# Kernel optimization log

Hardware: AMD Instinct MI355X
Metric: run time of the kernel (lower is better)

The kernel has to match this reference:

```python
import jax, jax.numpy as jnp
import numpy as np

N0, N1, N2 = 100000, 25000, 6250
E0, E1, E2 = 600000, 150000, 37500
K = 6


def cheb_conv(x, edge_index, W, b):
    """torch_geometric ChebConv with sym normalization, lambda_max=2:
    L_hat = -D^{-1/2} A D^{-1/2}; T0=x, T1=L_hat x, Tk=2 L_hat T_{k-1} - T_{k-2}."""
    n = x.shape[0]
    src, dst = edge_index[0], edge_index[1]
    deg = jax.ops.segment_sum(jnp.ones(src.shape[0], x.dtype), src, num_segments=n)
    dinv = jnp.where(deg > 0, jax.lax.rsqrt(jnp.maximum(deg, 1.0)), 0.0)
    w = -(dinv[src] * dinv[dst])  # [E]

    def prop(h):  # (L_hat h)_i = sum_{j->i} w_ij h_j
        return jax.ops.segment_sum(w[:, None] * h[src], dst, num_segments=n)

    Tx0 = x
    out = Tx0 @ W[0]
    Tx1 = prop(x)
    out = out + Tx1 @ W[1]
    for k in range(2, W.shape[0]):
        Tx2 = 2.0 * prop(Tx1) - Tx0
        out = out + Tx2 @ W[k]
        Tx0, Tx1 = Tx1, Tx2
    return out + b


def pool(x, rows, cols, vals, n_out):
    # sparse.mm(D, x): y[r] += v * x[c]
    return jax.ops.segment_sum(vals[:, None] * x[cols], rows, num_segments=n_out)


def setup_inputs() -> dict:
    key = jax.random.key(0)
    ks = jax.random.split(key, 16)
    inp = {}
    inp["x"] = jax.random.normal(ks[0], (N0, 3), jnp.float32)
    inp["edge_index0"] = jax.random.randint(ks[1], (2, E0), 0, N0, jnp.int32)
    inp["edge_index1"] = jax.random.randint(ks[2], (2, E1), 0, N1, jnp.int32)
    inp["edge_index2"] = jax.random.randint(ks[3], (2, E2), 0, N2, jnp.int32)
    s = 0.05
    inp["W0"] = jax.random.normal(ks[4], (K, 3, 128), jnp.float32) * s
    inp["b0"] = jax.random.normal(ks[5], (128,), jnp.float32) * s
    inp["W1"] = jax.random.normal(ks[6], (K, 128, 128), jnp.float32) * s
    inp["b1"] = jax.random.normal(ks[7], (128,), jnp.float32) * s
    inp["W2"] = jax.random.normal(ks[8], (K, 128, 256), jnp.float32) * s
    inp["b2"] = jax.random.normal(ks[9], (256,), jnp.float32) * s
    inp["D0_rows"] = jax.random.randint(ks[10], (100000,), 0, N1, jnp.int32)
    inp["D0_cols"] = jax.random.randint(ks[11], (100000,), 0, N0, jnp.int32)
    inp["D0_vals"] = jax.random.uniform(ks[12], (100000,), jnp.float32)
    inp["D1_rows"] = jax.random.randint(ks[13], (25000,), 0, N2, jnp.int32)
    inp["D1_cols"] = jax.random.randint(ks[14], (25000,), 0, N1, jnp.int32)
    inp["D1_vals"] = jax.random.uniform(ks[15], (25000,), jnp.float32)
    k2 = jax.random.split(jax.random.fold_in(key, 1), 2)
    inp["linW"] = jax.random.normal(k2[0], (10, N2 * 256), jnp.float32) * 0.001
    inp["linb"] = jax.random.normal(k2[1], (10,), jnp.float32) * s
    return inp


def reference(x, edge_index0, edge_index1, edge_index2, W0, b0, W1, b1, W2, b2,
              D0_rows, D0_cols, D0_vals, D1_rows, D1_cols, D1_vals, linW, linb):
    h = jax.nn.relu(cheb_conv(x, edge_index0, W0, b0))      # [N0,128]
    h = pool(h, D0_rows, D0_cols, D0_vals, N1)               # [N1,128]
    h = jax.nn.relu(cheb_conv(h, edge_index1, W1, b1))      # [N1,128]
    h = pool(h, D1_rows, D1_cols, D1_vals, N2)               # [N2,128]
    h = cheb_conv(h, edge_index2, W2, b2)                    # [N2,256]
    Z = linW @ h.reshape(-1) + linb                           # [10]
    return Z
```

## Files before the change

kernel.cpp:

```cpp
#include <hip/hip_runtime.h>


namespace {
constexpr int cN0 = 100000, cN1 = 25000, cN2 = 6250;
constexpr int cE0 = 600000, cE1 = 150000, cE2 = 37500;
constexpr int cD  = cN2 * 256;

constexpr int JN[8]  = {cN0, cN1, cN2, cN1, cN2, cN0, cN1, cN2};
constexpr int JE[8]  = {cE0, cE1, cE2, 100000, 25000, cE0, cE1, cE2};
constexpr int JB[8]  = {391, 98, 25, 98, 25, 391, 98, 25};
constexpr int JBBASE[9] = {0, 391, 489, 514, 612, 637, 1028, 1126, 1151};
constexpr int TB = 1151;
constexpr int JCB[8] = {293, 74, 19, 49, 13, 293, 74, 19};
constexpr int JCBASE[9] = {0, 293, 367, 386, 435, 448, 741, 815, 834};
constexpr int TCB = 834;
constexpr int CHUNK = 2048;
constexpr int BSTRIDE = 400;

constexpr int EBASE[5]   = {0, 600000, 750000, 787500, 887500};
constexpr int E_TOTAL    = 912500;
constexpr int SBASE[3]   = {0, 600000, 750000};
constexpr int S_TOTAL    = 787500;
constexpr int NBASE[5]   = {0, 100096, 125184, 131584, 156672};
constexpr int NPAD_TOTAL = 163072;
constexpr int DEGBASE[3] = {0, 100000, 125000};
constexpr int DEG_TOTAL  = 131250;
}

typedef __attribute__((ext_vector_type(8))) short short8;
typedef __attribute__((ext_vector_type(4))) float floatx4;

__device__ inline ushort f2bf(float f) {
  union { float f; unsigned u; } v; v.f = f;
  unsigned u = v.u;
  return (ushort)((u + 0x7FFFu + ((u >> 16) & 1u)) >> 16);
}

__device__ inline int job_of_cb(int cb) {
  int j = 0;
  while (cb >= JCBASE[j + 1]) ++j;
  return j;
}
__device__ inline int job_of_bucket(int g) {
  int j = 0;
  while (g >= JBBASE[j + 1]) ++j;
  return j;
}

__global__ __launch_bounds__(256) void c1_count_kernel(
    const int* __restrict__ k0, const int* __restrict__ k1, const int* __restrict__ k2,
    const int* __restrict__ k3, const int* __restrict__ k4, const int* __restrict__ k5,
    const int* __restrict__ k6, const int* __restrict__ k7,
    int* __restrict__ cntCB) {
  __shared__ int cnt[BSTRIDE];
  int cb = blockIdx.x;
  int j = job_of_cb(cb);
  int lb = cb - JCBASE[j];
  const int* keys;
  switch (j) {
    case 0: keys = k0; break; case 1: keys = k1; break; case 2: keys = k2; break;
    case 3: keys = k3; break; case 4: keys = k4; break; case 5: keys = k5; break;
    case 6: keys = k6; break; default: keys = k7; break;
  }
  int nB = JB[j];
  for (int b = threadIdx.x; b < nB; b += 256) cnt[b] = 0;
  __syncthreads();
  int e0 = lb * CHUNK;
  int e1 = min(e0 + CHUNK, JE[j]);
  for (int e = e0 + threadIdx.x; e < e1; e += 256)
    atomicAdd(&cnt[keys[e] >> 8], 1);
  __syncthreads();
  for (int b = threadIdx.x; b < nB; b += 256)
    cntCB[cb * BSTRIDE + b] = cnt[b];
}

__global__ __launch_bounds__(256) void c2a_scan_kernel(int* __restrict__ cntCB,
                                                       int* __restrict__ bucketTot) {
  __shared__ int s[256];
  int g = blockIdx.x;
  int j = job_of_bucket(g);
  int b = g - JBBASE[j];
  int cb0 = JCBASE[j], nCB = JCB[j];
  int carry = 0;
  for (int c0 = 0; c0 < nCB; c0 += 256) {
    int i = c0 + threadIdx.x;
    int v = (i < nCB) ? cntCB[(cb0 + i) * BSTRIDE + b] : 0;
    s[threadIdx.x] = v;
    __syncthreads();
    for (int d = 1; d < 256; d <<= 1) {
      int t = (threadIdx.x >= d) ? s[threadIdx.x - d] : 0;
      __syncthreads();
      s[threadIdx.x] += t;
      __syncthreads();
    }
    if (i < nCB) cntCB[(cb0 + i) * BSTRIDE + b] = carry + s[threadIdx.x] - v;
    carry += s[255];
    __syncthreads();
  }
  if (threadIdx.x == 0) bucketTot[g] = carry;
}

__global__ __launch_bounds__(256) void c2b_scan_kernel(const int* __restrict__ bucketTot,
                                                       int* __restrict__ bucketBase) {
  __shared__ int s[256];
  int j = blockIdx.x;
  int g0 = JBBASE[j], nB = JB[j];
  int carry = 0;
  for (int c0 = 0; c0 < nB; c0 += 256) {
    int i = c0 + threadIdx.x;
    int v = (i < nB) ? bucketTot[g0 + i] : 0;
    s[threadIdx.x] = v;
    __syncthreads();
    for (int d = 1; d < 256; d <<= 1) {
      int t = (threadIdx.x >= d) ? s[threadIdx.x - d] : 0;
      __syncthreads();
      s[threadIdx.x] += t;
      __syncthreads();
    }
    if (i < nB) bucketBase[g0 + i] = carry + s[threadIdx.x] - v;
    carry += s[255];
    __syncthreads();
  }
}

__global__ __launch_bounds__(256) void c3_src_kernel(
    const int* __restrict__ s0, const int* __restrict__ s1, const int* __restrict__ s2,
    const int* __restrict__ cntCB, const int* __restrict__ bucketBase,
    int* __restrict__ scatSrc) {
  __shared__ int base[BSTRIDE];
  int cb = blockIdx.x + JCBASE[5];
  int j = job_of_cb(cb);
  int lb = cb - JCBASE[j];
  const int* keys = (j == 5) ? s0 : (j == 6) ? s1 : s2;
  int nB = JB[j];
  for (int b = threadIdx.x; b < nB; b += 256)
    base[b] = SBASE[j - 5] + bucketBase[JBBASE[j] + b] + cntCB[cb * BSTRIDE + b];
  __syncthreads();
  int e0 = lb * CHUNK;
  int e1 = min(e0 + CHUNK, JE[j]);
  for (int e = e0 + threadIdx.x; e < e1; e += 256) {
    int s = keys[e];
    int pos = atomicAdd(&base[s >> 8], 1);
    scatSrc[pos] = s & 255;
  }
}

__global__ __launch_bounds__(256) void ddeg_kernel(const int* __restrict__ scatSrc,
                                                   const int* __restrict__ bucketTot,
                                                   const int* __restrict__ bucketBase,
                                                   float* __restrict__ dinv) {
  __shared__ int cnt[256];
  int g = blockIdx.x + JBBASE[5];
  int j = job_of_bucket(g);
  int b = g - JBBASE[j];
  int st = SBASE[j - 5] + bucketBase[g];
  int en = st + bucketTot[g];
  cnt[threadIdx.x] = 0;
  __syncthreads();
  for (int idx = st + threadIdx.x; idx < en; idx += 256)
    atomicAdd(&cnt[scatSrc[idx]], 1);
  __syncthreads();
  int node = b * 256 + threadIdx.x;
  if (node < JN[j]) {
    int c = cnt[threadIdx.x];
    dinv[DEGBASE[j - 5] + node] = (c > 0) ? rsqrtf((float)c) : 0.f;
  }
}

__global__ __launch_bounds__(256) void c3_dst_kernel(
    const int* __restrict__ d0, const int* __restrict__ s0,
    const int* __restrict__ d1, const int* __restrict__ s1,
    const int* __restrict__ d2, const int* __restrict__ s2,
    const int* __restrict__ p0r, const int* __restrict__ p0c, const float* __restrict__ p0v,
    const int* __restrict__ p1r, const int* __restrict__ p1c, const float* __restrict__ p1v,
    const float* __restrict__ dinv,
    const int* __restrict__ cntCB, const int* __restrict__ bucketBase,
    int2* __restrict__ scatPairs) {
  __shared__ int base[BSTRIDE];
  int cb = blockIdx.x;
  int j = job_of_cb(cb);
  int lb = cb - JCBASE[j];
  const int* dk; const int* sk; const float* vv = nullptr;
  switch (j) {
    case 0: dk = d0; sk = s0; break;
    case 1: dk = d1; sk = s1; break;
    case 2: dk = d2; sk = s2; break;
    case 3: dk = p0r; sk = p0c; vv = p0v; break;
    default: dk = p1r; sk = p1c; vv = p1v; break;
  }
  int nB = JB[j];
  for (int b = threadIdx.x; b < nB; b += 256)
    base[b] = EBASE[j] + bucketBase[JBBASE[j] + b] + cntCB[cb * BSTRIDE + b];
  __syncthreads();
  int e0 = lb * CHUNK;
  int e1 = min(e0 + CHUNK, JE[j]);
  for (int e = e0 + threadIdx.x; e < e1; e += 256) {
    int d = dk[e];
    int s = sk[e];
    float w;
    if (j < 3) w = -(dinv[DEGBASE[j] + s] * dinv[DEGBASE[j] + d]);
    else w = vv[e];
    int pos = atomicAdd(&base[d >> 8], 1);
    scatPairs[pos] = make_int2(((d & 255) << 17) | s, __float_as_int(w));
  }
}

__global__ __launch_bounds__(256) void dcsr_kernel(const int2* __restrict__ scatPairs,
                                                   const int* __restrict__ bucketTot,
                                                   const int* __restrict__ bucketBase,
                                                   int* __restrict__ off,
                                                   int2* __restrict__ csrPairs) {
  __shared__ int cnt[256];
  __shared__ int sArr[256];
  __shared__ int cur[256];
  int g = blockIdx.x;
  int j = job_of_bucket(g);
  int b = g - JBBASE[j];
  int relBase = bucketBase[g];
  int st = EBASE[j] + relBase;
  int en = st + bucketTot[g];
  cnt[threadIdx.x] = 0;
  __syncthreads();
  for (int idx = st + threadIdx.x; idx < en; idx += 256)
    atomicAdd(&cnt[scatPairs[idx].x >> 17], 1);
  __syncthreads();
  int v = cnt[threadIdx.x];
  sArr[threadIdx.x] = v;
  __syncthreads();
  for (int d = 1; d < 256; d <<= 1) {
    int t = (threadIdx.x >= d) ? sArr[threadIdx.x - d] : 0;
    __syncthreads();
    sArr[threadIdx.x] += t;
    __syncthreads();
  }
  int excl = sArr[threadIdx.x] - v;
  int node = b * 256 + threadIdx.x;
  if (node < JN[j]) off[NBASE[j] + node] = relBase + excl;
  if (threadIdx.x == 0 && b == JB[j] - 1) off[NBASE[j] + JN[j]] = JE[j];
  cur[threadIdx.x] = st + excl;
  __syncthreads();
  for (int idx = st + threadIdx.x; idx < en; idx += 256) {
    int2 p = scatPairs[idx];
    int dl = p.x >> 17;
    int s = p.x & 0x1FFFF;
    int pos = atomicAdd(&cur[dl], 1);
    csrPairs[pos] = make_int2(s, p.y);
  }
}

__global__ __launch_bounds__(256) void csr_prop128_kernel(
    const int* __restrict__ off, const int2* __restrict__ pairs,
    const float* __restrict__ h, float* __restrict__ y, ushort* __restrict__ ybf,
    const float* __restrict__ prev, float scale, int N) {
  int r = blockIdx.x * 8 + (threadIdx.x >> 5);
  int l = threadIdx.x & 31;
  if (r >= N) return;
  int s = off[r], e = off[r + 1];
  const float4* h4 = (const float4*)h;
  float ax = 0.f, ay = 0.f, az = 0.f, aw = 0.f;
  int j = s;
  for (; j + 4 <= e; j += 4) {
    int2 p0 = pairs[j], p1 = pairs[j + 1], p2 = pairs[j + 2], p3 = pairs[j + 3];
    float4 v0 = h4[(size_t)p0.x * 32 + l];
    float4 v1 = h4[(size_t)p1.x * 32 + l];
    float4 v2 = h4[(size_t)p2.x * 32 + l];
    float4 v3 = h4[(size_t)p3.x * 32 + l];
    float w0 = __int_as_float(p0.y), w1 = __int_as_float(p1.y);
    float w2 = __int_as_float(p2.y), w3 = __int_as_float(p3.y);
    ax += w0 * v0.x + w1 * v1.x + w2 * v2.x + w3 * v3.x;
    ay += w0 * v0.y + w1 * v1.y + w2 * v2.y + w3 * v3.y;
    az += w0 * v0.z + w1 * v1.z + w2 * v2.z + w3 * v3.z;
    aw += w0 * v0.w + w1 * v1.w + w2 * v2.w + w3 * v3.w;
  }
  for (; j < e; ++j) {
    int2 p = pairs[j];
    float4 v0 = h4[(size_t)p.x * 32 + l];
    float w = __int_as_float(p.y);
    ax += w * v0.x; ay += w * v0.y; az += w * v0.z; aw += w * v0.w;
  }
  float4 v = make_float4(scale * ax, scale * ay, scale * az, scale * aw);
  if (prev) {
    float4 pv = ((const float4*)prev)[(size_t)r * 32 + l];
    v.x -= pv.x; v.y -= pv.y; v.z -= pv.z; v.w -= pv.w;
  }
  if (y) ((float4*)y)[(size_t)r * 32 + l] = v;
  uint2 sp = make_uint2(f2bf(v.x) | ((unsigned)f2bf(v.y) << 16),
                        f2bf(v.z) | ((unsigned)f2bf(v.w) << 16));
  ((uint2*)ybf)[(size_t)r * 32 + l] = sp;
}

__global__ void csr_prop3_kernel(const int* __restrict__ off, const int2* __restrict__ pairs,
                                 const float4* __restrict__ T, float4* __restrict__ Tout,
                                 int kin, int kout, int kprev, float scale, int N) {
  int r = blockIdx.x * blockDim.x + threadIdx.x;
  if (r >= N) return;
  int s = off[r], e = off[r + 1];
  float ax = 0.f, ay = 0.f, az = 0.f;
  int j = s;
  for (; j + 4 <= e; j += 4) {
    int2 p0 = pairs[j], p1 = pairs[j + 1], p2 = pairs[j + 2], p3 = pairs[j + 3];
    float4 h0 = T[(size_t)p0.x * 6 + kin];
    float4 h1 = T[(size_t)p1.x * 6 + kin];
    float4 h2 = T[(size_t)p2.x * 6 + kin];
    float4 h3 = T[(size_t)p3.x * 6 + kin];
    float w0 = __int_as_float(p0.y), w1 = __int_as_float(p1.y);
    float w2 = __int_as_float(p2.y), w3 = __int_as_float(p3.y);
    ax += w0 * h0.x + w1 * h1.x + w2 * h2.x + w3 * h3.x;
    ay += w0 * h0.y + w1 * h1.y + w2 * h2.y + w3 * h3.y;
    az += w0 * h0.z + w1 * h1.z + w2 * h2.z + w3 * h3.z;
  }
  for (; j < e; ++j) {
    int2 p = pairs[j];
    float4 hv = T[(size_t)p.x * 6 + kin];
    float w = __int_as_float(p.y);
    ax += w * hv.x; ay += w * hv.y; az += w * hv.z;
  }
  float4 v = make_float4(scale * ax, scale * ay, scale * az, 0.f);
  if (kprev >= 0) {
    float4 pv = T[(size_t)r * 6 + kprev];
    v.x -= pv.x; v.y -= pv.y; v.z -= pv.z;
  }
  Tout[(size_t)r * 6 + kout] = v;
}

__global__ void copyx_kernel(const float* __restrict__ x, float4* __restrict__ Tb, int N) {
  int r = blockIdx.x * 256 + threadIdx.x;
  if (r < N) Tb[(size_t)r * 6] = make_float4(x[3 * r], x[3 * r + 1], x[3 * r + 2], 0.f);
}

__global__ __launch_bounds__(256) void g18pool_kernel(
    const int* __restrict__ off, const int2* __restrict__ pairs,
    const float4* __restrict__ Tb0, const float* __restrict__ W0,
    const float* __restrict__ b0, float* __restrict__ T0out,
    ushort* __restrict__ T0bf, int N) {
  int r = blockIdx.x * 2 + (threadIdx.x >> 7);
  int f = threadIdx.x & 127;
  float wcol[18];
#pragma unroll
  for (int t = 0; t < 18; ++t) wcol[t] = W0[t * 128 + f];
  float bv = b0[f];
  if (r >= N) return;
  int s = off[r], e = off[r + 1];
  float acc = 0.f;
  int j = s;
  for (; j + 2 <= e; j += 2) {
    int2 p0 = pairs[j], p1 = pairs[j + 1];
    const float4* t0 = Tb0 + (size_t)p0.x * 6;
    const float4* t1 = Tb0 + (size_t)p1.x * 6;
    float d0 = bv, d1 = bv;
#pragma unroll
    for (int k = 0; k < 6; ++k) {
      float4 a = t0[k];
      float4 b = t1[k];
      d0 += a.x * wcol[k * 3] + a.y * wcol[k * 3 + 1] + a.z * wcol[k * 3 + 2];
      d1 += b.x * wcol[k * 3] + b.y * wcol[k * 3 + 1] + b.z * wcol[k * 3 + 2];
    }
    acc += __int_as_float(p0.y) * fmaxf(d0, 0.f) + __int_as_float(p1.y) * fmaxf(d1, 0.f);
  }
  if (j < e) {
    int2 p = pairs[j];
    const float4* t0 = Tb0 + (size_t)p.x * 6;
    float d = bv;
#pragma unroll
    for (int k = 0; k < 6; ++k) {
      float4 a = t0[k];
      d += a.x * wcol[k * 3] + a.y * wcol[k * 3 + 1] + a.z * wcol[k * 3 + 2];
    }
    acc += __int_as_float(p.y) * fmaxf(d, 0.f);
  }
  T0out[(size_t)r * 128 + f] = acc;
  T0bf[(size_t)r * 128 + f] = f2bf(acc);
}

__global__ void prep_w_kernel(const float* __restrict__ W1, const float* __restrict__ W2,
                              ushort* __restrict__ Wt1, ushort* __restrict__ Wt2) {
  int i = blockIdx.x * 256 + threadIdx.x;
  if (i < 768 * 128) {
    int k = i / 128, n = i - k * 128;
    Wt1[(size_t)n * 768 + k] = f2bf(W1[i]);
  } else {
    int i2 = i - 768 * 128;
    if (i2 < 768 * 256) {
      int k = i2 / 256, n = i2 - k * 256;
      Wt2[(size_t)n * 768 + k] = f2bf(W2[i2]);
    }
  }
}

template <int RELU>
__global__ __launch_bounds__(256, 2) void gemm_mfma_kernel(
    const ushort* __restrict__ Tbf, const ushort* __restrict__ Wt,
    const float* __restrict__ bias, float* __restrict__ C, int M, int N) {
  __shared__ ushort Al[64][40];
  __shared__ ushort Bl[128][40];
  const int tid = threadIdx.x;
  const int rowBase = blockIdx.x * 64;
  const int colBase = blockIdx.y * 128;
  const int wave = tid >> 6;
  const int lane = tid & 63;
  const int m16 = lane & 15;
  const int quad = lane >> 4;
  const size_t Mstride = (size_t)M * 128;

  floatx4 acc[8];
#pragma unroll
  for (int c = 0; c < 8; ++c)
#pragma unroll
    for (int r = 0; r < 4; ++r) acc[c][r] = 0.f;

  const int sRow = tid >> 2;
  const int sK8 = (tid & 3) * 8;
  const int growA = rowBase + sRow;
  const bool aValid = growA < M;

  for (int kc = 0; kc < 24; ++kc) {
    uint4 av = make_uint4(0, 0, 0, 0);
    if (aValid)
      av = *(const uint4*)(Tbf + (size_t)(kc >> 2) * Mstride + (size_t)growA * 128
                           + ((kc & 3) << 5) + sK8);
    *(uint4*)&Al[sRow][sK8] = av;
#pragma unroll
    for (int l = 0; l < 2; ++l) {
      int lin = tid + l * 256;
      int bRow = lin >> 2;
      int bK8 = (lin & 3) * 8;
      *(uint4*)&Bl[bRow][bK8] =
          *(const uint4*)(Wt + (size_t)(colBase + bRow) * 768 + kc * 32 + bK8);
    }
    __syncthreads();

    short8 a = *(const short8*)&Al[wave * 16 + m16][quad * 8];
#pragma unroll
    for (int c = 0; c < 8; ++c) {
      short8 b = *(const short8*)&Bl[c * 16 + m16][quad * 8];
      acc[c] = __builtin_amdgcn_mfma_f32_16x16x32_bf16(a, b, acc[c], 0, 0, 0);
    }
    __syncthreads();
  }

#pragma unroll
  for (int c = 0; c < 8; ++c) {
    int col = colBase + c * 16 + m16;
    float bv = bias[col];
#pragma unroll
    for (int r = 0; r < 4; ++r) {
      int row = rowBase + wave * 16 + quad * 4 + r;
      if (row < M) {
        float v = acc[c][r] + bv;
        if (RELU) v = fmaxf(v, 0.f);
        C[(size_t)row * N + col] = v;
      }
    }
  }
}

__global__ void initout_kernel(float* __restrict__ out, const float* __restrict__ linb) {
  int i = threadIdx.x;
  if (i < 10) out[i] = linb[i];
}

__global__ __launch_bounds__(256) void linear_kernel(const float* __restrict__ Wl,
                                                     const float* __restrict__ h,
                                                     float* __restrict__ out, int D) {
  float p[10];
#pragma unroll
  for (int j = 0; j < 10; ++j) p[j] = 0.f;
  int stride = gridDim.x * blockDim.x;
  for (int i = blockIdx.x * blockDim.x + threadIdx.x; i < D; i += stride) {
    float hv = h[i];
#pragma unroll
    for (int j = 0; j < 10; ++j) p[j] += Wl[(size_t)j * D + i] * hv;
  }
#pragma unroll
  for (int j = 0; j < 10; ++j) {
#pragma unroll
    for (int off = 32; off > 0; off >>= 1) p[j] += __shfl_down(p[j], off, 64);
  }
  __shared__ float s[4][10];
  int wave = threadIdx.x >> 6, lane = threadIdx.x & 63;
  if (lane == 0) {
#pragma unroll
    for (int j = 0; j < 10; ++j) s[wave][j] = p[j];
  }
  __syncthreads();
  if (threadIdx.x < 10) {
    float t = s[0][threadIdx.x] + s[1][threadIdx.x] + s[2][threadIdx.x] + s[3][threadIdx.x];
    atomicAdd(&out[threadIdx.x], t);
  }
}

extern "C" void kernel_launch(void* const* d_in, const int* in_sizes, int n_in,
                              void* d_out, int out_size, void* d_ws, size_t ws_size,
                              hipStream_t stream) {
  const float* x    = (const float*)d_in[0];
  const int*   ei0  = (const int*)d_in[1];
  const int*   ei1  = (const int*)d_in[2];
  const int*   ei2  = (const int*)d_in[3];
  const float* W0   = (const float*)d_in[4];
  const float* b0   = (const float*)d_in[5];
  const float* W1   = (const float*)d_in[6];
  const float* b1   = (const float*)d_in[7];
  const float* W2   = (const float*)d_in[8];
  const float* b2   = (const float*)d_in[9];
  const int*   D0r  = (const int*)d_in[10];
  const int*   D0c  = (const int*)d_in[11];
  const float* D0v  = (const float*)d_in[12];
  const int*   D1r  = (const int*)d_in[13];
  const int*   D1c  = (const int*)d_in[14];
  const float* D1v  = (const float*)d_in[15];
  const float* linW = (const float*)d_in[16];
  const float* linb = (const float*)d_in[17];
  float* out = (float*)d_out;
  (void)in_sizes; (void)n_in; (void)out_size; (void)ws_size;

  const int* src0 = ei0;            const int* dst0 = ei0 + cE0;
  const int* src1 = ei1;            const int* dst1 = ei1 + cE1;
  const int* src2 = ei2;            const int* dst2 = ei2 + cE2;

  float* ws = (float*)d_ws;
  size_t off = 0;
  auto alloc = [&](size_t n) {
    float* p = ws + off;
    off += (n + 63) & ~size_t(63);
    return p;
  };
  float* dinv       = alloc(DEG_TOTAL);
  int*   cntCB      = (int*)alloc((size_t)TCB * BSTRIDE);
  int*   bucketTot  = (int*)alloc(TB);
  int*   bucketBase = (int*)alloc(TB);
  int*   scatSrc    = (int*)alloc(S_TOTAL);
  int2*  scatPairs  = (int2*)alloc((size_t)2 * E_TOTAL);
  int2*  csrPairs   = (int2*)alloc((size_t)2 * E_TOTAL);
  int*   offArr     = (int*)alloc(NPAD_TOTAL);
  ushort* Wt1       = (ushort*)alloc(768 * 128 / 2);
  ushort* Wt2       = (ushort*)alloc(768 * 256 / 2);
  float4* Tb0       = (float4*)alloc((size_t)cN0 * 24);
  float* Tlvl1      = alloc((size_t)6 * cN1 * 128);
  ushort* Tbf1      = (ushort*)alloc((size_t)6 * cN1 * 64);
  float* out1       = alloc((size_t)cN1 * 128);
  float* Tlvl2      = alloc((size_t)6 * cN2 * 128);
  ushort* Tbf2      = (ushort*)alloc((size_t)6 * cN2 * 64);
  float* out2       = alloc((size_t)cN2 * 256);

  auto nb = [](long long n) { return (unsigned)((n + 255) / 256); };

  c1_count_kernel<<<TCB, 256, 0, stream>>>(dst0, dst1, dst2, D0r, D1r,
                                           src0, src1, src2, cntCB);
  c2a_scan_kernel<<<TB, 256, 0, stream>>>(cntCB, bucketTot);
  c2b_scan_kernel<<<8, 256, 0, stream>>>(bucketTot, bucketBase);
  c3_src_kernel<<<TCB - JCBASE[5], 256, 0, stream>>>(src0, src1, src2,
                                                     cntCB, bucketBase, scatSrc);
  ddeg_kernel<<<TB - JBBASE[5], 256, 0, stream>>>(scatSrc, bucketTot, bucketBase, dinv);
  c3_dst_kernel<<<JCBASE[5], 256, 0, stream>>>(dst0, src0, dst1, src1, dst2, src2,
                                               D0r, D0c, D0v, D1r, D1c, D1v,
                                               dinv, cntCB, bucketBase, scatPairs);
  dcsr_kernel<<<JBBASE[5], 256, 0, stream>>>(scatPairs, bucketTot, bucketBase,
                                             offArr, csrPairs);
  prep_w_kernel<<<nb(768 * 384), 256, 0, stream>>>(W1, W2, Wt1, Wt2);

  auto seg_off   = [&](int s) { return offArr + NBASE[s]; };
  auto seg_pairs = [&](int s) { return csrPairs + EBASE[s]; };

  copyx_kernel<<<nb(cN0), 256, 0, stream>>>(x, Tb0, cN0);
  csr_prop3_kernel<<<nb(cN0), 256, 0, stream>>>(seg_off(0), seg_pairs(0),
      Tb0, Tb0, 0, 1, -1, 1.f, cN0);
  csr_prop3_kernel<<<nb(cN0), 256, 0, stream>>>(seg_off(0), seg_pairs(0),
      Tb0, Tb0, 1, 2, 0, 2.f, cN0);
  csr_prop3_kernel<<<nb(cN0), 256, 0, stream>>>(seg_off(0), seg_pairs(0),
      Tb0, Tb0, 2, 3, 1, 2.f, cN0);
  csr_prop3_kernel<<<nb(cN0), 256, 0, stream>>>(seg_off(0), seg_pairs(0),
      Tb0, Tb0, 3, 4, 2, 2.f, cN0);
  csr_prop3_kernel<<<nb(cN0), 256, 0, stream>>>(seg_off(0), seg_pairs(0),
      Tb0, Tb0, 4, 5, 3, 2.f, cN0);
  g18pool_kernel<<<(cN1 + 1) / 2, 256, 0, stream>>>(
      seg_off(3), seg_pairs(3), Tb0, W0, b0, Tlvl1, Tbf1, cN1);

  {
    auto Tk  = [&](int k) { return Tlvl1 + (size_t)k * cN1 * 128; };
    auto Tbk = [&](int k) { return Tbf1 + (size_t)k * cN1 * 128; };
    auto prop = [&](int kin, int kout, int kprev, float scale, bool needF32) {
      csr_prop128_kernel<<<(cN1 + 7) / 8, 256, 0, stream>>>(
          seg_off(1), seg_pairs(1), Tk(kin), needF32 ? Tk(kout) : nullptr, Tbk(kout),
          (kprev >= 0) ? Tk(kprev) : nullptr, scale, cN1);
    };
    prop(0, 1, -1, 1.f, true);
    prop(1, 2, 0, 2.f, true);
    prop(2, 3, 1, 2.f, true);
    prop(3, 4, 2, 2.f, true);
    prop(4, 5, 3, 2.f, false);
    dim3 g((cN1 + 63) / 64, 1);
    gemm_mfma_kernel<1><<<g, 256, 0, stream>>>(Tbf1, Wt1, b1, out1, cN1, 128);
  }

  csr_prop128_kernel<<<(cN2 + 7) / 8, 256, 0, stream>>>(
      seg_off(4), seg_pairs(4), out1, Tlvl2, Tbf2, nullptr, 1.f, cN2);

  {
    auto Tk  = [&](int k) { return Tlvl2 + (size_t)k * cN2 * 128; };
    auto Tbk = [&](int k) { return Tbf2 + (size_t)k * cN2 * 128; };
    auto prop = [&](int kin, int kout, int kprev, float scale, bool needF32) {
      csr_prop128_kernel<<<(cN2 + 7) / 8, 256, 0, stream>>>(
          seg_off(2), seg_pairs(2), Tk(kin), needF32 ? Tk(kout) : nullptr, Tbk(kout),
          (kprev >= 0) ? Tk(kprev) : nullptr, scale, cN2);
    };
    prop(0, 1, -1, 1.f, true);
    prop(1, 2, 0, 2.f, true);
    prop(2, 3, 1, 2.f, true);
    prop(3, 4, 2, 2.f, true);
    prop(4, 5, 3, 2.f, false);
    dim3 g((cN2 + 63) / 64, 2);
    gemm_mfma_kernel<0><<<g, 256, 0, stream>>>(Tbf2, Wt2, b2, out2, cN2, 256);
  }

  initout_kernel<<<1, 64, 0, stream>>>(out, linb);
  linear_kernel<<<512, 256, 0, stream>>>(linW, out2, out, cD);
}
```

Baseline: 494.0 us.

## Unfuse layer-0 dense+ReLU from pooling and store Chebyshev terms planar

The level-0 Chebyshev terms move from an interleaved [N,6] float4 layout to six separate planes of N float4. The fused gather-and-recompute pool kernel is replaced by a dense h0 kernel that materialises relu(T·W0+b0) for all 100k nodes, followed by the generic 128-wide CSR propagation kernel for pooling. This removes the redundant 18-term recompute for every pooling edge and the strided gathers of six float4 per edge. In exchange it writes and rereads a 51 MB h0 buffer and adds a kernel launch.

```diff
diff --git a/kernel.cpp b/kernel.cpp
--- a/kernel.cpp
+++ b/kernel.cpp
@@ -290,8 +290,8 @@
 }
 
 __global__ void csr_prop3_kernel(const int* __restrict__ off, const int2* __restrict__ pairs,
-                                 const float4* __restrict__ T, float4* __restrict__ Tout,
-                                 int kin, int kout, int kprev, float scale, int N) {
+                                 const float4* __restrict__ h, float4* __restrict__ y,
+                                 const float4* __restrict__ prev, float scale, int N) {
   int r = blockIdx.x * blockDim.x + threadIdx.x;
   if (r >= N) return;
   int s = off[r], e = off[r + 1];
@@ -299,10 +299,7 @@
   int j = s;
   for (; j + 4 <= e; j += 4) {
     int2 p0 = pairs[j], p1 = pairs[j + 1], p2 = pairs[j + 2], p3 = pairs[j + 3];
-    float4 h0 = T[(size_t)p0.x * 6 + kin];
-    float4 h1 = T[(size_t)p1.x * 6 + kin];
-    float4 h2 = T[(size_t)p2.x * 6 + kin];
-    float4 h3 = T[(size_t)p3.x * 6 + kin];
+    float4 h0 = h[p0.x], h1 = h[p1.x], h2 = h[p2.x], h3 = h[p3.x];
     float w0 = __int_as_float(p0.y), w1 = __int_as_float(p1.y);
     float w2 = __int_as_float(p2.y), w3 = __int_as_float(p3.y);
     ax += w0 * h0.x + w1 * h1.x + w2 * h2.x + w3 * h3.x;
@@ -311,65 +308,39 @@
   }
   for (; j < e; ++j) {
     int2 p = pairs[j];
-    float4 hv = T[(size_t)p.x * 6 + kin];
+    float4 hv = h[p.x];
     float w = __int_as_float(p.y);
     ax += w * hv.x; ay += w * hv.y; az += w * hv.z;
   }
   float4 v = make_float4(scale * ax, scale * ay, scale * az, 0.f);
-  if (kprev >= 0) {
-    float4 pv = T[(size_t)r * 6 + kprev];
+  if (prev) {
+    float4 pv = prev[r];
     v.x -= pv.x; v.y -= pv.y; v.z -= pv.z;
   }
-  Tout[(size_t)r * 6 + kout] = v;
+  y[r] = v;
 }
 
 __global__ void copyx_kernel(const float* __restrict__ x, float4* __restrict__ Tb, int N) {
   int r = blockIdx.x * 256 + threadIdx.x;
-  if (r < N) Tb[(size_t)r * 6] = make_float4(x[3 * r], x[3 * r + 1], x[3 * r + 2], 0.f);
-}
-
-__global__ __launch_bounds__(256) void g18pool_kernel(
-    const int* __restrict__ off, const int2* __restrict__ pairs,
+  if (r < N) Tb[r] = make_float4(x[3 * r], x[3 * r + 1], x[3 * r + 2], 0.f);
+}
+
+__global__ __launch_bounds__(256) void h0_kernel(
     const float4* __restrict__ Tb0, const float* __restrict__ W0,
-    const float* __restrict__ b0, float* __restrict__ T0out,
-    ushort* __restrict__ T0bf, int N) {
+    const float* __restrict__ b0, float* __restrict__ h0, int N0) {
   int r = blockIdx.x * 2 + (threadIdx.x >> 7);
   int f = threadIdx.x & 127;
   float wcol[18];
 #pragma unroll
   for (int t = 0; t < 18; ++t) wcol[t] = W0[t * 128 + f];
-  float bv = b0[f];
-  if (r >= N) return;
-  int s = off[r], e = off[r + 1];
-  float acc = 0.f;
-  int j = s;
-  for (; j + 2 <= e; j += 2) {
-    int2 p0 = pairs[j], p1 = pairs[j + 1];
-    const float4* t0 = Tb0 + (size_t)p0.x * 6;
-    const float4* t1 = Tb0 + (size_t)p1.x * 6;
-    float d0 = bv, d1 = bv;
-#pragma unroll
-    for (int k = 0; k < 6; ++k) {
-      float4 a = t0[k];
-      float4 b = t1[k];
-      d0 += a.x * wcol[k * 3] + a.y * wcol[k * 3 + 1] + a.z * wcol[k * 3 + 2];
-      d1 += b.x * wcol[k * 3] + b.y * wcol[k * 3 + 1] + b.z * wcol[k * 3 + 2];
-    }
-    acc += __int_as_float(p0.y) * fmaxf(d0, 0.f) + __int_as_float(p1.y) * fmaxf(d1, 0.f);
-  }
-  if (j < e) {
-    int2 p = pairs[j];
-    const float4* t0 = Tb0 + (size_t)p.x * 6;
-    float d = bv;
-#pragma unroll
-    for (int k = 0; k < 6; ++k) {
-      float4 a = t0[k];
-      d += a.x * wcol[k * 3] + a.y * wcol[k * 3 + 1] + a.z * wcol[k * 3 + 2];
-    }
-    acc += __int_as_float(p.y) * fmaxf(d, 0.f);
-  }
-  T0out[(size_t)r * 128 + f] = acc;
-  T0bf[(size_t)r * 128 + f] = f2bf(acc);
+  if (r >= N0) return;
+  float d = b0[f];
+#pragma unroll
+  for (int k = 0; k < 6; ++k) {
+    float4 t = Tb0[(size_t)k * N0 + r];
+    d += t.x * wcol[k * 3] + t.y * wcol[k * 3 + 1] + t.z * wcol[k * 3 + 2];
+  }
+  h0[(size_t)r * 128 + f] = fmaxf(d, 0.f);
 }
 
 __global__ void prep_w_kernel(const float* __restrict__ W1, const float* __restrict__ W2,
@@ -534,7 +505,8 @@
   int*   offArr     = (int*)alloc(NPAD_TOTAL);
   ushort* Wt1       = (ushort*)alloc(768 * 128 / 2);
   ushort* Wt2       = (ushort*)alloc(768 * 256 / 2);
-  float4* Tb0       = (float4*)alloc((size_t)cN0 * 24);
+  float4* Tb0       = (float4*)alloc((size_t)6 * cN0 * 4);
+  float* h0buf      = alloc((size_t)cN0 * 128);
   float* Tlvl1      = alloc((size_t)6 * cN1 * 128);
   ushort* Tbf1      = (ushort*)alloc((size_t)6 * cN1 * 64);
   float* out1       = alloc((size_t)cN1 * 128);
@@ -562,18 +534,22 @@
   auto seg_pairs = [&](int s) { return csrPairs + EBASE[s]; };
 
   copyx_kernel<<<nb(cN0), 256, 0, stream>>>(x, Tb0, cN0);
-  csr_prop3_kernel<<<nb(cN0), 256, 0, stream>>>(seg_off(0), seg_pairs(0),
-      Tb0, Tb0, 0, 1, -1, 1.f, cN0);
-  csr_prop3_kernel<<<nb(cN0), 256, 0, stream>>>(seg_off(0), seg_pairs(0),
-      Tb0, Tb0, 1, 2, 0, 2.f, cN0);
-  csr_prop3_kernel<<<nb(cN0), 256, 0, stream>>>(seg_off(0), seg_pairs(0),
-      Tb0, Tb0, 2, 3, 1, 2.f, cN0);
-  csr_prop3_kernel<<<nb(cN0), 256, 0, stream>>>(seg_off(0), seg_pairs(0),
-      Tb0, Tb0, 3, 4, 2, 2.f, cN0);
-  csr_prop3_kernel<<<nb(cN0), 256, 0, stream>>>(seg_off(0), seg_pairs(0),
-      Tb0, Tb0, 4, 5, 3, 2.f, cN0);
-  g18pool_kernel<<<(cN1 + 1) / 2, 256, 0, stream>>>(
-      seg_off(3), seg_pairs(3), Tb0, W0, b0, Tlvl1, Tbf1, cN1);
+  {
+    auto Tk = [&](int k) { return Tb0 + (size_t)k * cN0; };
+    csr_prop3_kernel<<<nb(cN0), 256, 0, stream>>>(seg_off(0), seg_pairs(0),
+        Tk(0), Tk(1), nullptr, 1.f, cN0);
+    csr_prop3_kernel<<<nb(cN0), 256, 0, stream>>>(seg_off(0), seg_pairs(0),
+        Tk(1), Tk(2), Tk(0), 2.f, cN0);
+    csr_prop3_kernel<<<nb(cN0), 256, 0, stream>>>(seg_off(0), seg_pairs(0),
+        Tk(2), Tk(3), Tk(1), 2.f, cN0);
+    csr_prop3_kernel<<<nb(cN0), 256, 0, stream>>>(seg_off(0), seg_pairs(0),
+        Tk(3), Tk(4), Tk(2), 2.f, cN0);
+    csr_prop3_kernel<<<nb(cN0), 256, 0, stream>>>(seg_off(0), seg_pairs(0),
+        Tk(4), Tk(5), Tk(3), 2.f, cN0);
+  }
+  h0_kernel<<<(cN0 + 1) / 2, 256, 0, stream>>>(Tb0, W0, b0, h0buf, cN0);
+  csr_prop128_kernel<<<(cN1 + 7) / 8, 256, 0, stream>>>(
+      seg_off(3), seg_pairs(3), h0buf, Tlvl1, Tbf1, nullptr, 1.f, cN1);
 
   {
     auto Tk  = [&](int k) { return Tlvl1 + (size_t)k * cN1 * 128; };
```

After: 481.2 us. 1.03x faster.
